# Kernel optimization log

Hardware: AMD Instinct MI355X
Metric: run time of the kernel (lower is better)

## Reference

```python
import jax, jax.numpy as jnp
import numpy as np

RADIUS = [1.0, 1.5, 2.0, 100.0]  # bucket boundaries; last is catch-all
NFILT = len(RADIUS)
C_IN, C_OUT = 256, 512


def setup_inputs() -> dict:
    key = jax.random.key(0)
    k1, k2, k3, k4 = jax.random.split(key, 4)
    b, n = 16, 4096
    feat = jax.random.normal(k1, (b, n, C_IN), dtype=jnp.float32)
    xyz = jax.random.normal(k2, (b, n, 3), dtype=jnp.float32)
    # init per original reset_parameters
    std = 2.0 * np.sqrt(2.0 / (C_IN + C_OUT))
    a = np.sqrt(3.0) * std
    weight = jax.random.uniform(k3, (NFILT, C_OUT, C_IN), dtype=jnp.float32, minval=-a, maxval=a)
    bound = 1.0 / np.sqrt(C_IN)
    bias = jax.random.uniform(k4, (NFILT, C_OUT), dtype=jnp.float32, minval=-bound, maxval=bound)
    return {"feat": feat, "xyz": xyz, "weight": weight, "bias": bias}


def reference(feat, xyz, weight, bias):
    b, n, c = feat.shape
    p = feat.reshape(b * n, c)                      # (P, C)
    radii = jnp.asarray(RADIUS, dtype=feat.dtype)
    r_norm = jnp.linalg.norm(xyz.reshape(b * n, 3), axis=1)
    # first radius with r_norm < r (same as the sequential break in map2filtId)
    filt_id = jnp.argmax(r_norm[:, None] < radii[None, :], axis=1)  # (P,)
    # grouped linear expressed densely: all Nfilt GEMMs, then per-point select
    all_out = jnp.einsum('pc,foc->fpo', p, weight) + bias[:, None, :]  # (F, P, O)
    out = jnp.take_along_axis(all_out, filt_id[None, :, None], axis=0)[0]  # (P, O)
    return out.reshape(b, n, -1)
```

## Files before the change

### kernel.cpp

```cpp
#include <hip/hip_runtime.h>
#include <hip/hip_bf16.h>

#define C_IN   256
#define C_OUT  512
#define NFILT  4

#define BM 128
#define BN 128
#define BK 32
#define SAS 40

#define NSTEP 8

typedef __attribute__((ext_vector_type(8))) short bf16x8;
typedef __attribute__((ext_vector_type(4))) float floatx4;

union Pack8 { uint4 u; __hip_bfloat16 h[8]; };

__global__ __launch_bounds__(1024) void bucketize_kernel(
    const float* __restrict__ xyz, int* __restrict__ idxbuf,
    int* __restrict__ cnt, int P)
{
    __shared__ int hist[NFILT];
    __shared__ int wbase[16][NFILT];
    __shared__ int gbase[NFILT];

    int tid = threadIdx.x;
    int wid = tid >> 6;
    int lane = tid & 63;
    if (tid < NFILT) hist[tid] = 0;
    __syncthreads();

    int pid = blockIdx.x * 1024 + tid;
    int filt = -1;
    if (pid < P) {
        float x = xyz[pid * 3 + 0];
        float y = xyz[pid * 3 + 1];
        float z = xyz[pid * 3 + 2];
        float r2 = __fadd_rn(__fadd_rn(__fmul_rn(x, x), __fmul_rn(y, y)), __fmul_rn(z, z));
        float r = sqrtf(r2);
        if (r < 1.0f)        filt = 0;
        else if (r < 1.5f)   filt = 1;
        else if (r < 2.0f)   filt = 2;
        else if (r < 100.0f) filt = 3;
        else                 filt = 0;
    }

    int myoff = 0;
#pragma unroll
    for (int f = 0; f < NFILT; ++f) {
        unsigned long long m = __ballot(filt == f);
        if (lane == 0) wbase[wid][f] = atomicAdd(&hist[f], (int)__popcll(m));
        if (filt == f) myoff = __popcll(m & ((1ull << lane) - 1ull));
    }
    __syncthreads();
    if (tid < NFILT) gbase[tid] = atomicAdd(&cnt[tid], hist[tid]);
    __syncthreads();

    if (filt >= 0)
        idxbuf[filt * P + gbase[filt] + wbase[wid][filt] + myoff] = pid;
}

__global__ void convert_w_kernel(const float* __restrict__ w,
                                 ushort* __restrict__ wb,
                                 int* __restrict__ cnt) {
    if (blockIdx.x == 0 && threadIdx.x < NFILT) cnt[threadIdx.x] = 0;
    int i = (blockIdx.x * blockDim.x + threadIdx.x) * 4;
    float4 v = *(const float4*)(w + i);
    union { ushort4 u; __hip_bfloat16 h[4]; } cv;
    cv.h[0] = __float2bfloat16(v.x);
    cv.h[1] = __float2bfloat16(v.y);
    cv.h[2] = __float2bfloat16(v.z);
    cv.h[3] = __float2bfloat16(v.w);
    *(ushort4*)(wb + i) = cv.u;
}

#define STAGE_AB(s, b) do {                                                     \
    int kByteA = (s) * 128;                                                     \
    int kByteB = (s) * 64;                                                      \
    _Pragma("unroll")                                                           \
    for (int n = 0; n < 4; ++n) {                                               \
        int seg = wid * 4 + n;                                                  \
        const char* srcA = (const char*)feat                                    \
            + ((size_t)sIdxv[n] * (C_IN * 4)) + kByteA + aschunk * 16;          \
        __builtin_amdgcn_global_load_lds(                                       \
            (const __attribute__((address_space(1))) void*)srcA,                \
            (__attribute__((address_space(3))) void*)&sAf[b][seg * 256], 16, 0, 0); \
    }                                                                           \
    _Pragma("unroll")                                                           \
    for (int n = 0; n < 2; ++n) {                                               \
        int seg = wid * 2 + n;                                                  \
        int row = seg * 16 + (lane >> 2);                                       \
        const char* srcB = bBase + ((size_t)(wRow0 + row) * (C_IN * 2))         \
                                 + kByteB + bschunk * 16;                       \
        __builtin_amdgcn_global_load_lds(                                       \
            (const __attribute__((address_space(1))) void*)srcB,                \
            (__attribute__((address_space(3))) void*)&sBb[b][seg * 512], 16, 0, 0); \
    }                                                                           \
} while (0)

__global__ __launch_bounds__(256, 2) void gemm_fast_kernel(
    const float* __restrict__ feat, const ushort* __restrict__ wb,
    const float* __restrict__ bias, const int* __restrict__ idxbuf,
    const int* __restrict__ cnt, float* __restrict__ out, int P)
{
    __shared__ float  sAf[3][BM * 32];
    __shared__ ushort sBb[3][BN * 32];
    __shared__ int    sIdx[BM];
    __shared__ float  sBias[BN];

    int lid = blockIdx.x + (blockIdx.y << 2);
    int g = lid & 7;
    int q = lid >> 3;
    int cTile = q & 3;
    int t = ((q >> 2) << 3) + g;

    int c0 = cnt[0], c1 = cnt[1], c2 = cnt[2], c3 = cnt[3];
    int counts[4] = {c0, c1, c2, c3};
    int f = -1, lt = 0;
    for (int ff = 0; ff < 4; ++ff) {
        int nt = (counts[ff] + BM - 1) / BM;
        if (t < nt) { f = ff; lt = t; break; }
        t -= nt;
    }
    if (f < 0) return;

    int tid = threadIdx.x;
    int oBase = cTile * BN;
    int cn = counts[f];
    int wRow0 = f * C_OUT + oBase;

    int wid = tid >> 6;
    int lane = tid & 63;
    int wm = (wid >> 1) * 64;
    int wn = (wid & 1) * 64;
    int lcol = lane & 15;
    int quad = lane >> 4;

    int am = lcol & 7;
    int rchunkB = (quad ^ ((lcol >> 1) & 3)) * 8;

    int aschunk = (lane & 7) ^ ((lane >> 3) & 7);
    int bschunk = (lane & 3) ^ ((lane >> 3) & 3);

    const char* bBase = (const char*)wb;

    if (tid < BM) {
        int r = lt * BM + tid;
        sIdx[tid] = (r < cn) ? idxbuf[f * P + r] : -1;
    }
    if (tid < BN) sBias[tid] = bias[f * C_OUT + oBase + tid];
    __syncthreads();

    int sIdxv[4];
#pragma unroll
    for (int n = 0; n < 4; ++n) {
        int r = wid * 32 + n * 8 + (lane >> 3);
        int v = sIdx[r];
        sIdxv[n] = (v < 0) ? 0 : v;
    }

    STAGE_AB(0, 0);
    STAGE_AB(1, 1);

    floatx4 acc[4][4];
#pragma unroll
    for (int i = 0; i < 4; ++i)
#pragma unroll
        for (int j = 0; j < 4; ++j)
            acc[i][j] = (floatx4){0.f, 0.f, 0.f, 0.f};

#pragma unroll
    for (int s = 0; s < NSTEP; ++s) {
        if (s < NSTEP - 1) asm volatile("s_waitcnt vmcnt(6)" ::: "memory");
        else               asm volatile("s_waitcnt vmcnt(0)" ::: "memory");
        __builtin_amdgcn_s_barrier();
        __builtin_amdgcn_sched_barrier(0);

        if (s + 2 < NSTEP) STAGE_AB(s + 2, (s + 2) % 3);

        const float*  cA = sAf[s % 3];
        const ushort* cB = sBb[s % 3];

        bf16x8 af[4], bfr[4];
#pragma unroll
        for (int i = 0; i < 4; ++i) {
            int r = wm + i * 16 + lcol;
            int p0 = (2 * quad) ^ am;
            int p1 = (2 * quad + 1) ^ am;
            float4 f0 = *(const float4*)&cA[r * 32 + p0 * 4];
            float4 f1 = *(const float4*)&cA[r * 32 + p1 * 4];
            Pack8 pk;
            pk.h[0] = __float2bfloat16(f0.x); pk.h[1] = __float2bfloat16(f0.y);
            pk.h[2] = __float2bfloat16(f0.z); pk.h[3] = __float2bfloat16(f0.w);
            pk.h[4] = __float2bfloat16(f1.x); pk.h[5] = __float2bfloat16(f1.y);
            pk.h[6] = __float2bfloat16(f1.z); pk.h[7] = __float2bfloat16(f1.w);
            af[i] = *reinterpret_cast<bf16x8*>(&pk);
        }
#pragma unroll
        for (int j = 0; j < 4; ++j)
            bfr[j] = *(const bf16x8*)&cB[(wn + j * 16 + lcol) * 32 + rchunkB];
#pragma unroll
        for (int i = 0; i < 4; ++i)
#pragma unroll
            for (int j = 0; j < 4; ++j)
                acc[i][j] = __builtin_amdgcn_mfma_f32_16x16x32_bf16(af[i], bfr[j], acc[i][j], 0, 0, 0);
    }

#pragma unroll
    for (int i = 0; i < 4; ++i) {
        int r0 = wm + i * 16 + quad * 4;
        int pid0 = sIdx[r0 + 0];
        int pid1 = sIdx[r0 + 1];
        int pid2 = sIdx[r0 + 2];
        int pid3 = sIdx[r0 + 3];
#pragma unroll
        for (int j = 0; j < 4; ++j) {
            int o = oBase + wn + j * 16 + lcol;
            float bv = sBias[wn + j * 16 + lcol];
            if (pid0 >= 0) out[pid0 * C_OUT + o] = acc[i][j][0] + bv;
            if (pid1 >= 0) out[pid1 * C_OUT + o] = acc[i][j][1] + bv;
            if (pid2 >= 0) out[pid2 * C_OUT + o] = acc[i][j][2] + bv;
            if (pid3 >= 0) out[pid3 * C_OUT + o] = acc[i][j][3] + bv;
        }
    }
}

__global__ __launch_bounds__(256) void gemm_kernel(
    const float* __restrict__ feat, const ushort* __restrict__ wb,
    const float* __restrict__ bias, const int* __restrict__ idxbuf,
    const int* __restrict__ cnt, float* __restrict__ out, int P)
{
    __shared__ ushort sA[BM * SAS];
    __shared__ ushort sB[BN * SAS];
    __shared__ int    sIdx[BM];
    __shared__ float  sBias[BN];

    int lid = blockIdx.x + (blockIdx.y << 2);
    int g = lid & 7;
    int q = lid >> 3;
    int cTile = q & 3;
    int t = ((q >> 2) << 3) + g;

    int counts[4];
    counts[0] = cnt[0]; counts[1] = cnt[1]; counts[2] = cnt[2]; counts[3] = cnt[3];
    int f = -1, lt = 0;
    for (int ff = 0; ff < 4; ++ff) {
        int nt = (counts[ff] + BM - 1) / BM;
        if (t < nt) { f = ff; lt = t; break; }
        t -= nt;
    }
    if (f < 0) return;

    int tid = threadIdx.x;
    int oBase = cTile * BN;
    int rowBase = lt * BM;
    int cn = counts[f];

    if (tid < BM) {
        int r = rowBase + tid;
        sIdx[tid] = (r < cn) ? idxbuf[f * P + r] : -1;
    }
    if (tid < BN) sBias[tid] = bias[f * C_OUT + oBase + tid];
    __syncthreads();

    int sRow = tid >> 1;
    int sHalf = tid & 1;
    int myIdx = sIdx[sRow];
    const float* aRow = feat + (size_t)(myIdx < 0 ? 0 : myIdx) * C_IN + sHalf * 16;
    const ushort* bRow = wb + (size_t)(f * C_OUT + oBase + sRow) * C_IN + sHalf * 16;

    int wid = tid >> 6;
    int lane = tid & 63;
    int wm = (wid >> 1) * 64;
    int wn = (wid & 1) * 64;
    int lcol = lane & 15;
    int quad = lane >> 4;

    floatx4 acc[4][4];
#pragma unroll
    for (int i = 0; i < 4; ++i)
#pragma unroll
        for (int j = 0; j < 4; ++j)
            acc[i][j] = (floatx4){0.f, 0.f, 0.f, 0.f};

    for (int kk = 0; kk < C_IN; kk += BK) {
        const float* ap = aRow + kk;
        float4 a0 = *(const float4*)(ap + 0);
        float4 a1 = *(const float4*)(ap + 4);
        float4 a2 = *(const float4*)(ap + 8);
        float4 a3 = *(const float4*)(ap + 12);
        const ushort* bp = bRow + kk;
        uint4 b01 = *(const uint4*)(bp + 0);
        uint4 b23 = *(const uint4*)(bp + 8);

        Pack8 p0, p1;
        p0.h[0] = __float2bfloat16(a0.x); p0.h[1] = __float2bfloat16(a0.y);
        p0.h[2] = __float2bfloat16(a0.z); p0.h[3] = __float2bfloat16(a0.w);
        p0.h[4] = __float2bfloat16(a1.x); p0.h[5] = __float2bfloat16(a1.y);
        p0.h[6] = __float2bfloat16(a1.z); p0.h[7] = __float2bfloat16(a1.w);
        p1.h[0] = __float2bfloat16(a2.x); p1.h[1] = __float2bfloat16(a2.y);
        p1.h[2] = __float2bfloat16(a2.z); p1.h[3] = __float2bfloat16(a2.w);
        p1.h[4] = __float2bfloat16(a3.x); p1.h[5] = __float2bfloat16(a3.y);
        p1.h[6] = __float2bfloat16(a3.z); p1.h[7] = __float2bfloat16(a3.w);

        ushort* dA = &sA[sRow * SAS + sHalf * 16];
        *(uint4*)(dA + 0) = p0.u;
        *(uint4*)(dA + 8) = p1.u;
        ushort* dB = &sB[sRow * SAS + sHalf * 16];
        *(uint4*)(dB + 0) = b01;
        *(uint4*)(dB + 8) = b23;

        __syncthreads();

        bf16x8 af[4], bfr[4];
#pragma unroll
        for (int i = 0; i < 4; ++i)
            af[i] = *(const bf16x8*)&sA[(wm + i * 16 + lcol) * SAS + quad * 8];
#pragma unroll
        for (int j = 0; j < 4; ++j)
            bfr[j] = *(const bf16x8*)&sB[(wn + j * 16 + lcol) * SAS + quad * 8];
#pragma unroll
        for (int i = 0; i < 4; ++i)
#pragma unroll
            for (int j = 0; j < 4; ++j)
                acc[i][j] = __builtin_amdgcn_mfma_f32_16x16x32_bf16(af[i], bfr[j], acc[i][j], 0, 0, 0);

        __syncthreads();
    }

#pragma unroll
    for (int i = 0; i < 4; ++i) {
        int r0 = wm + i * 16 + quad * 4;
        int pid0 = sIdx[r0 + 0];
        int pid1 = sIdx[r0 + 1];
        int pid2 = sIdx[r0 + 2];
        int pid3 = sIdx[r0 + 3];
#pragma unroll
        for (int j = 0; j < 4; ++j) {
            int o = oBase + wn + j * 16 + lcol;
            float bv = sBias[wn + j * 16 + lcol];
            if (pid0 >= 0) out[pid0 * C_OUT + o] = acc[i][j][0] + bv;
            if (pid1 >= 0) out[pid1 * C_OUT + o] = acc[i][j][1] + bv;
            if (pid2 >= 0) out[pid2 * C_OUT + o] = acc[i][j][2] + bv;
            if (pid3 >= 0) out[pid3 * C_OUT + o] = acc[i][j][3] + bv;
        }
    }
}

extern "C" void kernel_launch(void* const* d_in, const int* in_sizes, int n_in,
                              void* d_out, int out_size, void* d_ws, size_t ws_size,
                              hipStream_t stream) {
    const float* feat = (const float*)d_in[0];
    const float* xyz  = (const float*)d_in[1];
    const float* w    = (const float*)d_in[2];
    const float* bias = (const float*)d_in[3];
    float* out = (float*)d_out;
    int P = in_sizes[0] / C_IN;

    char* ws = (char*)d_ws;
    size_t offIdx = 0;
    size_t offCnt = (size_t)4 * P * 4;
    size_t offWb  = offCnt + 16;
    size_t needed = offWb + (size_t)NFILT * C_OUT * C_IN * 2;

    int* idxbuf = (int*)(ws + offIdx);
    int* cntp   = (int*)(ws + offCnt);
    ushort* wb  = (ushort*)(ws + offWb);

    convert_w_kernel<<<(NFILT * C_OUT * C_IN) / 1024, 256, 0, stream>>>(w, wb, cntp);
    bucketize_kernel<<<(P + 1023) / 1024, 1024, 0, stream>>>(xyz, idxbuf, cntp, P);

    int tilesY = ((P / BM + NFILT + 7) / 8) * 8;
    dim3 grid(C_OUT / BN, tilesY);

    if (ws_size >= needed) {
        gemm_fast_kernel<<<grid, 256, 0, stream>>>(feat, wb, bias, idxbuf, cntp, out, P);
    } else {
        gemm_kernel<<<grid, 256, 0, stream>>>(feat, wb, bias, idxbuf, cntp, out, P);
    }
}
```

Measured before the change: 239.0 us.

## Cover full output width per block with 1024-thread single-buffered GEMM

Restructures the gathered GEMM so each 1024-thread block computes a 128-point by full 512-output tile, loading each gathered feature row only once instead of four times across output tiles. Features are converted to bf16 when stored to shared memory rather than at fragment-load time. The triple-buffered async global_load_lds pipeline is replaced by plain register loads with two barriers per K step, so load/compute overlap now relies on occupancy across blocks. The grid shrinks to one dimension of point tiles, reducing block count and possibly parallelism.

```diff
diff --git a/kernel.cpp b/kernel.cpp
--- a/kernel.cpp
+++ b/kernel.cpp
@@ -10,7 +10,7 @@
 #define BK 32
 #define SAS 40
 
-#define NSTEP 8
+#define ST 36
 
 typedef __attribute__((ext_vector_type(8))) short bf16x8;
 typedef __attribute__((ext_vector_type(4))) float floatx4;
@@ -75,48 +75,18 @@
     *(ushort4*)(wb + i) = cv.u;
 }
 
-#define STAGE_AB(s, b) do {                                                     \
-    int kByteA = (s) * 128;                                                     \
-    int kByteB = (s) * 64;                                                      \
-    _Pragma("unroll")                                                           \
-    for (int n = 0; n < 4; ++n) {                                               \
-        int seg = wid * 4 + n;                                                  \
-        const char* srcA = (const char*)feat                                    \
-            + ((size_t)sIdxv[n] * (C_IN * 4)) + kByteA + aschunk * 16;          \
-        __builtin_amdgcn_global_load_lds(                                       \
-            (const __attribute__((address_space(1))) void*)srcA,                \
-            (__attribute__((address_space(3))) void*)&sAf[b][seg * 256], 16, 0, 0); \
-    }                                                                           \
-    _Pragma("unroll")                                                           \
-    for (int n = 0; n < 2; ++n) {                                               \
-        int seg = wid * 2 + n;                                                  \
-        int row = seg * 16 + (lane >> 2);                                       \
-        const char* srcB = bBase + ((size_t)(wRow0 + row) * (C_IN * 2))         \
-                                 + kByteB + bschunk * 16;                       \
-        __builtin_amdgcn_global_load_lds(                                       \
-            (const __attribute__((address_space(1))) void*)srcB,                \
-            (__attribute__((address_space(3))) void*)&sBb[b][seg * 512], 16, 0, 0); \
-    }                                                                           \
-} while (0)
-
-__global__ __launch_bounds__(256, 2) void gemm_fast_kernel(
+__global__ __launch_bounds__(1024, 4) void gemm_fast_kernel(
     const float* __restrict__ feat, const ushort* __restrict__ wb,
     const float* __restrict__ bias, const int* __restrict__ idxbuf,
     const int* __restrict__ cnt, float* __restrict__ out, int P)
 {
-    __shared__ float  sAf[3][BM * 32];
-    __shared__ ushort sBb[3][BN * 32];
+    __shared__ ushort sA[BM * ST];
+    __shared__ ushort sB[C_OUT * ST];
     __shared__ int    sIdx[BM];
-    __shared__ float  sBias[BN];
-
-    int lid = blockIdx.x + (blockIdx.y << 2);
-    int g = lid & 7;
-    int q = lid >> 3;
-    int cTile = q & 3;
-    int t = ((q >> 2) << 3) + g;
-
-    int c0 = cnt[0], c1 = cnt[1], c2 = cnt[2], c3 = cnt[3];
-    int counts[4] = {c0, c1, c2, c3};
+    __shared__ float  sBias[C_OUT];
+
+    int t = blockIdx.x;
+    int counts[4] = {cnt[0], cnt[1], cnt[2], cnt[3]};
     int f = -1, lt = 0;
     for (int ff = 0; ff < 4; ++ff) {
         int nt = (counts[ff] + BM - 1) / BM;
@@ -126,102 +96,79 @@
     if (f < 0) return;
 
     int tid = threadIdx.x;
-    int oBase = cTile * BN;
     int cn = counts[f];
-    int wRow0 = f * C_OUT + oBase;
-
-    int wid = tid >> 6;
-    int lane = tid & 63;
-    int wm = (wid >> 1) * 64;
-    int wn = (wid & 1) * 64;
-    int lcol = lane & 15;
-    int quad = lane >> 4;
-
-    int am = lcol & 7;
-    int rchunkB = (quad ^ ((lcol >> 1) & 3)) * 8;
-
-    int aschunk = (lane & 7) ^ ((lane >> 3) & 7);
-    int bschunk = (lane & 3) ^ ((lane >> 3) & 3);
-
-    const char* bBase = (const char*)wb;
 
     if (tid < BM) {
         int r = lt * BM + tid;
         sIdx[tid] = (r < cn) ? idxbuf[f * P + r] : -1;
     }
-    if (tid < BN) sBias[tid] = bias[f * C_OUT + oBase + tid];
-    __syncthreads();
-
-    int sIdxv[4];
-#pragma unroll
-    for (int n = 0; n < 4; ++n) {
-        int r = wid * 32 + n * 8 + (lane >> 3);
-        int v = sIdx[r];
-        sIdxv[n] = (v < 0) ? 0 : v;
-    }
-
-    STAGE_AB(0, 0);
-    STAGE_AB(1, 1);
-
-    floatx4 acc[4][4];
-#pragma unroll
-    for (int i = 0; i < 4; ++i)
-#pragma unroll
-        for (int j = 0; j < 4; ++j)
+    if (tid < C_OUT) sBias[tid] = bias[f * C_OUT + tid];
+    __syncthreads();
+
+    int ar = tid >> 3, aq = tid & 7;
+    int ap = sIdx[ar]; if (ap < 0) ap = 0;
+    const float* aSrc = feat + (size_t)ap * C_IN + aq * 4;
+    int bc = tid >> 1, bh = tid & 1;
+    const ushort* bSrc = wb + (size_t)(f * C_OUT + bc) * C_IN + bh * 16;
+
+    int wid = tid >> 6, lane = tid & 63;
+    int wm = (wid >> 2) * 32;
+    int wn = (wid & 3) * 128;
+    int lcol = lane & 15, quad = lane >> 4;
+
+    floatx4 acc[2][8];
+#pragma unroll
+    for (int i = 0; i < 2; ++i)
+#pragma unroll
+        for (int j = 0; j < 8; ++j)
             acc[i][j] = (floatx4){0.f, 0.f, 0.f, 0.f};
 
-#pragma unroll
-    for (int s = 0; s < NSTEP; ++s) {
-        if (s < NSTEP - 1) asm volatile("s_waitcnt vmcnt(6)" ::: "memory");
-        else               asm volatile("s_waitcnt vmcnt(0)" ::: "memory");
-        __builtin_amdgcn_s_barrier();
-        __builtin_amdgcn_sched_barrier(0);
-
-        if (s + 2 < NSTEP) STAGE_AB(s + 2, (s + 2) % 3);
-
-        const float*  cA = sAf[s % 3];
-        const ushort* cB = sBb[s % 3];
-
-        bf16x8 af[4], bfr[4];
-#pragma unroll
-        for (int i = 0; i < 4; ++i) {
-            int r = wm + i * 16 + lcol;
-            int p0 = (2 * quad) ^ am;
-            int p1 = (2 * quad + 1) ^ am;
-            float4 f0 = *(const float4*)&cA[r * 32 + p0 * 4];
-            float4 f1 = *(const float4*)&cA[r * 32 + p1 * 4];
-            Pack8 pk;
-            pk.h[0] = __float2bfloat16(f0.x); pk.h[1] = __float2bfloat16(f0.y);
-            pk.h[2] = __float2bfloat16(f0.z); pk.h[3] = __float2bfloat16(f0.w);
-            pk.h[4] = __float2bfloat16(f1.x); pk.h[5] = __float2bfloat16(f1.y);
-            pk.h[6] = __float2bfloat16(f1.z); pk.h[7] = __float2bfloat16(f1.w);
-            af[i] = *reinterpret_cast<bf16x8*>(&pk);
+    for (int kk = 0; kk < C_IN; kk += BK) {
+        float4 av = *(const float4*)(aSrc + kk);
+        union { ushort4 u; __hip_bfloat16 h[4]; } cv;
+        cv.h[0] = __float2bfloat16(av.x);
+        cv.h[1] = __float2bfloat16(av.y);
+        cv.h[2] = __float2bfloat16(av.z);
+        cv.h[3] = __float2bfloat16(av.w);
+        *(ushort4*)&sA[ar * ST + aq * 4] = cv.u;
+        uint4 b0 = *(const uint4*)(bSrc + kk);
+        uint4 b1 = *(const uint4*)(bSrc + kk + 8);
+        *(uint4*)&sB[bc * ST + bh * 16 + 0] = b0;
+        *(uint4*)&sB[bc * ST + bh * 16 + 8] = b1;
+        __syncthreads();
+
+        bf16x8 a0 = *(const bf16x8*)&sA[(wm + 0  + lcol) * ST + quad * 8];
+        bf16x8 a1 = *(const bf16x8*)&sA[(wm + 16 + lcol) * ST + quad * 8];
+#pragma unroll
+        for (int jh = 0; jh < 2; ++jh) {
+            bf16x8 bf[4];
+#pragma unroll
+            for (int j = 0; j < 4; ++j)
+                bf[j] = *(const bf16x8*)&sB[(wn + (jh * 4 + j) * 16 + lcol) * ST + quad * 8];
+#pragma unroll
+            for (int j = 0; j < 4; ++j) {
+                acc[0][jh * 4 + j] = __builtin_amdgcn_mfma_f32_16x16x32_bf16(a0, bf[j], acc[0][jh * 4 + j], 0, 0, 0);
+                acc[1][jh * 4 + j] = __builtin_amdgcn_mfma_f32_16x16x32_bf16(a1, bf[j], acc[1][jh * 4 + j], 0, 0, 0);
+            }
         }
-#pragma unroll
-        for (int j = 0; j < 4; ++j)
-            bfr[j] = *(const bf16x8*)&cB[(wn + j * 16 + lcol) * 32 + rchunkB];
-#pragma unroll
-        for (int i = 0; i < 4; ++i)
-#pragma unroll
-            for (int j = 0; j < 4; ++j)
-                acc[i][j] = __builtin_amdgcn_mfma_f32_16x16x32_bf16(af[i], bfr[j], acc[i][j], 0, 0, 0);
-    }
-
-#pragma unroll
-    for (int i = 0; i < 4; ++i) {
+        __syncthreads();
+    }
+
+#pragma unroll
+    for (int i = 0; i < 2; ++i) {
         int r0 = wm + i * 16 + quad * 4;
-        int pid0 = sIdx[r0 + 0];
-        int pid1 = sIdx[r0 + 1];
-        int pid2 = sIdx[r0 + 2];
-        int pid3 = sIdx[r0 + 3];
-#pragma unroll
-        for (int j = 0; j < 4; ++j) {
-            int o = oBase + wn + j * 16 + lcol;
-            float bv = sBias[wn + j * 16 + lcol];
-            if (pid0 >= 0) out[pid0 * C_OUT + o] = acc[i][j][0] + bv;
-            if (pid1 >= 0) out[pid1 * C_OUT + o] = acc[i][j][1] + bv;
-            if (pid2 >= 0) out[pid2 * C_OUT + o] = acc[i][j][2] + bv;
-            if (pid3 >= 0) out[pid3 * C_OUT + o] = acc[i][j][3] + bv;
+        int p0 = sIdx[r0 + 0];
+        int p1 = sIdx[r0 + 1];
+        int p2 = sIdx[r0 + 2];
+        int p3 = sIdx[r0 + 3];
+#pragma unroll
+        for (int j = 0; j < 8; ++j) {
+            int o = wn + j * 16 + lcol;
+            float bv = sBias[o];
+            if (p0 >= 0) out[(size_t)p0 * C_OUT + o] = acc[i][j][0] + bv;
+            if (p1 >= 0) out[(size_t)p1 * C_OUT + o] = acc[i][j][1] + bv;
+            if (p2 >= 0) out[(size_t)p2 * C_OUT + o] = acc[i][j][2] + bv;
+            if (p3 >= 0) out[(size_t)p3 * C_OUT + o] = acc[i][j][3] + bv;
         }
     }
 }
@@ -371,12 +318,12 @@
     convert_w_kernel<<<(NFILT * C_OUT * C_IN) / 1024, 256, 0, stream>>>(w, wb, cntp);
     bucketize_kernel<<<(P + 1023) / 1024, 1024, 0, stream>>>(xyz, idxbuf, cntp, P);
 
-    int tilesY = ((P / BM + NFILT + 7) / 8) * 8;
-    dim3 grid(C_OUT / BN, tilesY);
-
     if (ws_size >= needed) {
-        gemm_fast_kernel<<<grid, 256, 0, stream>>>(feat, wb, bias, idxbuf, cntp, out, P);
+        int tiles = P / BM + NFILT;
+        gemm_fast_kernel<<<tiles, 1024, 0, stream>>>(feat, wb, bias, idxbuf, cntp, out, P);
     } else {
+        int tilesY = ((P / BM + NFILT + 7) / 8) * 8;
+        dim3 grid(C_OUT / BN, tilesY);
         gemm_kernel<<<grid, 256, 0, stream>>>(feat, wb, bias, idxbuf, cntp, out, P);
     }
 }
```

Measured after the change: 236.6 us. Within noise of the previous version (-1.0%).
